# Performance work log

Hardware: AMD Instinct MI355X
Metric: run time of the kernel (lower is better)

## Reference

```python
import jax, jax.numpy as jnp
import numpy as np

M = 16            # num_frequencies
DIM = 512         # dim_input
B = 32768         # flattened batch
H = M + 1         # raw complex table side
N = 2 * M + 1     # autocorrelated table side
NPAR = H * H      # (m+1)^2


def setup_inputs() -> dict:
    key = jax.random.key(0)
    k1, k2, k3 = jax.random.split(key, 3)
    inputs = jax.random.normal(k1, (B, DIM), dtype=jnp.float32)
    targets = jax.random.uniform(k2, (B, 2), dtype=jnp.float32)  # points in [0,1) subset of [-1,1]^2
    # nn.init.normal_(weight, 0.01) => mean=0.01, std=1.0 ; bias zeros
    W = jax.random.normal(k3, (2 * NPAR, DIM), dtype=jnp.float32) + 0.01
    b = jnp.zeros((2 * NPAR,), dtype=jnp.float32)
    return {"inputs": inputs, "targets": targets, "W": W, "b": b}


def reference(inputs, targets, W, b):
    # Linear -> unconstrained complex (m+1)x(m+1) table per sample
    p = inputs @ W.T + b                                   # (B, 2*NPAR)
    real = p[:, :NPAR].reshape(-1, H, H)
    imag = p[:, NPAR:].reshape(-1, H, H)
    seq = jax.lax.complex(real, imag)                      # (B, H, H) complex64

    # 2D linear autocorrelation r[tau] = sum_i seq[i+tau] * conj(seq[i]),
    # tau in [-M, M]^2, via zero-padded FFT (equivalent to the grouped conv2d).
    F = jnp.fft.fft2(seq, s=(N, N))                        # (B, N, N)
    ac = jnp.fft.ifft2(F * jnp.conj(F))                    # circular autocorr
    ac = jnp.roll(ac, (M, M), axis=(-2, -1))               # index a -> lag a-M

    # Normalize so C[0,0] (= centre) equals 1/4 => unit mass on [-1,1]^2
    centre = ac[:, M, M].real                              # sum |seq|^2 > 0
    C = ac / (4.0 * centre)[:, None, None]                 # (B, N, N)

    # Evaluate f(x,y) = sum_{kx,ky} C * exp(i*pi*(kx*x + ky*y))
    k = jnp.arange(-M, M + 1, dtype=jnp.float32)
    kx, ky = jnp.meshgrid(k, k, indexing='xy')             # (N, N)
    tx = targets[:, 0][:, None, None]
    ty = targets[:, 1][:, None, None]
    phase = kx[None] * tx + ky[None] * ty                  # (B, N, N)
    exps = jnp.exp(1j * jnp.pi * phase)
    pdf = jnp.einsum('bij,bij->b', C, exps).real           # (B,)
    return pdf
```

## Files before the change

kernel.cpp:

```cpp
#include <hip/hip_runtime.h>

#define NPARC 289
#define NOUT  578
#define DIMK  512
#define BATCH 32768

typedef __bf16 bf16x8 __attribute__((ext_vector_type(8)));
typedef float floatx4 __attribute__((ext_vector_type(4)));

__device__ __forceinline__ unsigned short f2bf(float f) {
    unsigned u = __float_as_uint(f);
    u = (u + 0x7fffu + ((u >> 16) & 1u)) >> 16;
    return (unsigned short)u;
}

__global__ void prep_w(const float* __restrict__ W, unsigned short* __restrict__ Wp) {
    int wid = threadIdx.x >> 6;
    int lane = threadIdx.x & 63;
    int slot = blockIdx.x * 4 + wid;
    int k = lane * 8;
    unsigned short v[8];
    if (slot < NOUT) {
        int o = (slot & 1) ? NPARC + (slot >> 1) : (slot >> 1);
        const float* src = W + (size_t)o * DIMK + k;
        #pragma unroll
        for (int j = 0; j < 8; ++j) v[j] = f2bf(src[j]);
    } else {
        #pragma unroll
        for (int j = 0; j < 8; ++j) v[j] = 0;
    }
    int ct = slot >> 4;
    int ks = k >> 5;
    int ln = (((k >> 3) & 3) << 4) + (slot & 15);
    uint4 o4;
    o4.x = (unsigned)v[0] | ((unsigned)v[1] << 16);
    o4.y = (unsigned)v[2] | ((unsigned)v[3] << 16);
    o4.z = (unsigned)v[4] | ((unsigned)v[5] << 16);
    o4.w = (unsigned)v[6] | ((unsigned)v[7] << 16);
    *(uint4*)(Wp + (size_t)((ct * 16 + ks) * 64 + ln) * 8) = o4;
}

__global__ __launch_bounds__(512, 2) void fused_kernel(
    const float* __restrict__ inputs, const float* __restrict__ targets,
    const float* __restrict__ bias, const unsigned short* __restrict__ Wp,
    float* __restrict__ out)
{
    __shared__ __align__(16) float buf[2][64 * 128];
    __shared__ float R[8][64][3];
    const int tid  = threadIdx.x;
    const int base = blockIdx.x * 64;
    const int wid  = tid >> 6;
    const int lane = tid & 63;
    const int quad = lane >> 4;
    const int lcol = lane & 15;
    const int ct0  = wid * 5;
    const bf16x8* Wf = (const bf16x8*)Wp;

#define STAGE(nb, kt) do {                                                    \
    _Pragma("unroll") for (int j_ = 0; j_ < 4; ++j_) {                        \
        int I_ = wid * 4 + j_;                                                \
        int r_ = I_ * 2 + (lane >> 5);                                        \
        int cl_ = (lane & 31) ^ (r_ & 15);                                    \
        const float* g_ = inputs + (size_t)(base + r_) * DIMK + (kt) * 128 + cl_ * 4; \
        void* l_ = (char*)&buf[nb][0] + I_ * 1024;                            \
        __builtin_amdgcn_global_load_lds(                                     \
            (const __attribute__((address_space(1))) unsigned int*)g_,        \
            (__attribute__((address_space(3))) unsigned int*)l_, 16, 0, 0);   \
    }                                                                         \
} while (0)

#define LDRAW(R_, nb, kl) do {                                                \
    _Pragma("unroll") for (int st_ = 0; st_ < 4; ++st_) {                     \
        int s_ = st_ * 16 + lcol;                                             \
        int cb_ = (kl) * 8 + quad * 2;                                        \
        const char* p_ = (const char*)&buf[nb][0] + s_ * 512;                 \
        R_[2 * st_]     = *(const floatx4*)(p_ + ((cb_)     ^ (s_ & 15)) * 16); \
        R_[2 * st_ + 1] = *(const floatx4*)(p_ + ((cb_ + 1) ^ (s_ & 15)) * 16); \
    }                                                                         \
} while (0)

#define LDAW(dst, ksg)                                                        \
    { _Pragma("unroll") for (int t5_ = 0; t5_ < 5; ++t5_)                     \
        dst[t5_] = Wf[((size_t)(ct0 + t5_) * 16 + (ksg)) * 64 + lane]; }

#define KS(nb, ksg, RU, RP, PF, AWU, AWP) do {                                \
    if (PF) LDRAW(RP, nb, ((ksg) & 3) + 1);                                   \
    if ((ksg) < 15) LDAW(AWP, (ksg) + 1);                                     \
    bf16x8 bsv[4];                                                            \
    _Pragma("unroll") for (int st_ = 0; st_ < 4; ++st_) {                     \
        union { __bf16 h[8]; bf16x8 v; } cu_;                                 \
        cu_.h[0] = (__bf16)RU[2 * st_][0];     cu_.h[1] = (__bf16)RU[2 * st_][1]; \
        cu_.h[2] = (__bf16)RU[2 * st_][2];     cu_.h[3] = (__bf16)RU[2 * st_][3]; \
        cu_.h[4] = (__bf16)RU[2 * st_ + 1][0]; cu_.h[5] = (__bf16)RU[2 * st_ + 1][1]; \
        cu_.h[6] = (__bf16)RU[2 * st_ + 1][2]; cu_.h[7] = (__bf16)RU[2 * st_ + 1][3]; \
        bsv[st_] = cu_.v;                                                     \
    }                                                                         \
    __builtin_amdgcn_sched_barrier(0);                                        \
    __builtin_amdgcn_s_setprio(1);                                            \
    _Pragma("unroll") for (int t5_ = 0; t5_ < 5; ++t5_)                       \
        { _Pragma("unroll") for (int st_ = 0; st_ < 4; ++st_)                 \
            acc[t5_][st_] = __builtin_amdgcn_mfma_f32_16x16x32_bf16(          \
                AWU[t5_], bsv[st_], acc[t5_][st_], 0, 0, 0); }                \
    __builtin_amdgcn_s_setprio(0);                                            \
    __builtin_amdgcn_sched_barrier(0);                                        \
} while (0)

    floatx4 acc[5][4];
    #pragma unroll
    for (int t5 = 0; t5 < 5; ++t5)
        #pragma unroll
        for (int st = 0; st < 4; ++st) acc[t5][st] = (floatx4){0.f, 0.f, 0.f, 0.f};

    bf16x8 aw0[5], aw1[5];
    floatx4 rA[8], rB[8];

    STAGE(0, 0);
    LDAW(aw0, 0);
    __syncthreads();

    STAGE(1, 1);
    LDRAW(rA, 0, 0);
    KS(0, 0,  rA, rB, 1, aw0, aw1);
    KS(0, 1,  rB, rA, 1, aw1, aw0);
    KS(0, 2,  rA, rB, 1, aw0, aw1);
    KS(0, 3,  rB, rA, 0, aw1, aw0);
    __syncthreads();

    STAGE(0, 2);
    LDRAW(rA, 1, 0);
    KS(1, 4,  rA, rB, 1, aw0, aw1);
    KS(1, 5,  rB, rA, 1, aw1, aw0);
    KS(1, 6,  rA, rB, 1, aw0, aw1);
    KS(1, 7,  rB, rA, 0, aw1, aw0);
    __syncthreads();

    STAGE(1, 3);
    LDRAW(rA, 0, 0);
    KS(0, 8,  rA, rB, 1, aw0, aw1);
    KS(0, 9,  rB, rA, 1, aw1, aw0);
    KS(0, 10, rA, rB, 1, aw0, aw1);
    KS(0, 11, rB, rA, 0, aw1, aw0);
    __syncthreads();

    LDRAW(rA, 1, 0);
    KS(1, 12, rA, rB, 1, aw0, aw1);
    KS(1, 13, rB, rA, 1, aw1, aw0);
    KS(1, 14, rA, rB, 1, aw0, aw1);
    KS(1, 15, rB, rA, 0, aw1, aw0);

    float xs[4], ys[4];
    #pragma unroll
    for (int st = 0; st < 4; ++st) {
        float2 t2 = *(const float2*)(targets + 2 * (base + st * 16 + lcol));
        xs[st] = 0.5f * t2.x;
        ys[st] = 0.5f * t2.y;
    }

    float pd[4]  = {0.f, 0.f, 0.f, 0.f};
    float pr[4]  = {0.f, 0.f, 0.f, 0.f};
    float pim[4] = {0.f, 0.f, 0.f, 0.f};

    #pragma unroll
    for (int t5 = 0; t5 < 5; ++t5)
        #pragma unroll
        for (int p = 0; p < 2; ++p) {
            int colw = (ct0 + t5) * 16 + quad * 4 + 2 * p;
            if (colw < NOUT) {
                int jj = colw >> 1;
                int r = jj / 17;
                int c = jj - r * 17;
                float cf = (float)c, rf = (float)r;
                float be = bias[jj];
                float bo = bias[jj + NPARC];
                #pragma unroll
                for (int st = 0; st < 4; ++st) {
                    float ve = acc[t5][st][2 * p]     + be;
                    float vo = acc[t5][st][2 * p + 1] + bo;
                    float u = fmaf(cf, xs[st], rf * ys[st]);
                    u = __builtin_amdgcn_fractf(u);
                    float sn = __builtin_amdgcn_sinf(u);
                    float cs = __builtin_amdgcn_cosf(u);
                    pd[st]  = fmaf(ve, ve, pd[st]);
                    pd[st]  = fmaf(vo, vo, pd[st]);
                    pr[st]  = fmaf(ve, cs, pr[st]);
                    pr[st]  = fmaf(-vo, sn, pr[st]);
                    pim[st] = fmaf(ve, sn, pim[st]);
                    pim[st] = fmaf(vo, cs, pim[st]);
                }
            }
        }

    #pragma unroll
    for (int d = 16; d < 64; d <<= 1)
        #pragma unroll
        for (int st = 0; st < 4; ++st) {
            pd[st]  += __shfl_xor(pd[st], d, 64);
            pr[st]  += __shfl_xor(pr[st], d, 64);
            pim[st] += __shfl_xor(pim[st], d, 64);
        }

    if (lane < 16) {
        #pragma unroll
        for (int st = 0; st < 4; ++st) {
            int sl = st * 16 + lane;
            R[wid][sl][0] = pd[st];
            R[wid][sl][1] = pr[st];
            R[wid][sl][2] = pim[st];
        }
    }
    __syncthreads();

    if (tid < 64) {
        float sd = 0.f, sr = 0.f, si = 0.f;
        #pragma unroll
        for (int w = 0; w < 8; ++w) {
            sd += R[w][tid][0];
            sr += R[w][tid][1];
            si += R[w][tid][2];
        }
        out[base + tid] = (sr * sr + si * si) / (4.0f * sd);
    }
#undef STAGE
#undef LDRAW
#undef LDAW
#undef KS
}

extern "C" void kernel_launch(void* const* d_in, const int* in_sizes, int n_in,
                              void* d_out, int out_size, void* d_ws, size_t ws_size,
                              hipStream_t stream) {
    const float* inputs  = (const float*)d_in[0];
    const float* targets = (const float*)d_in[1];
    const float* W       = (const float*)d_in[2];
    const float* bias    = (const float*)d_in[3];
    unsigned short* Wp   = (unsigned short*)d_ws;

    prep_w<<<160, 256, 0, stream>>>(W, Wp);
    fused_kernel<<<BATCH / 64, 512, 0, stream>>>(inputs, targets, bias, Wp, (float*)d_out);
}
```

Baseline: 120.3 us.

## Stage inputs as bf16 in LDS via register prefetch and triple-buffered weights

Replaces the async global-to-LDS fp32 copy with register-staged global loads that convert the input tile to bf16 once per block before writing it to a half-size swizzled LDS buffer. MFMA operand reads then become single bf16x8 LDS loads with no per-step conversion, and weight fragments rotate through three register sets to prefetch two k-steps ahead. It also uses explicit lgkmcnt waits plus raw s_barrier in place of __syncthreads. The intent is to halve LDS footprint and traffic and remove redundant fp32-to-bf16 conversions done by every wave, at the cost of more VGPRs for the prefetched global data and extra weight buffers.

```diff
diff --git a/kernel.cpp b/kernel.cpp
--- a/kernel.cpp
+++ b/kernel.cpp
@@ -45,7 +45,7 @@
     const float* __restrict__ bias, const unsigned short* __restrict__ Wp,
     float* __restrict__ out)
 {
-    __shared__ __align__(16) float buf[2][64 * 128];
+    __shared__ __align__(16) unsigned short buf[2][1024][8];
     __shared__ float R[8][64][3];
     const int tid  = threadIdx.x;
     const int base = blockIdx.x * 64;
@@ -56,54 +56,62 @@
     const int ct0  = wid * 5;
     const bf16x8* Wf = (const bf16x8*)Wp;
 
-#define STAGE(nb, kt) do {                                                    \
-    _Pragma("unroll") for (int j_ = 0; j_ < 4; ++j_) {                        \
-        int I_ = wid * 4 + j_;                                                \
-        int r_ = I_ * 2 + (lane >> 5);                                        \
-        int cl_ = (lane & 31) ^ (r_ & 15);                                    \
-        const float* g_ = inputs + (size_t)(base + r_) * DIMK + (kt) * 128 + cl_ * 4; \
-        void* l_ = (char*)&buf[nb][0] + I_ * 1024;                            \
-        __builtin_amdgcn_global_load_lds(                                     \
-            (const __attribute__((address_space(1))) unsigned int*)g_,        \
-            (__attribute__((address_space(3))) unsigned int*)l_, 16, 0, 0);   \
-    }                                                                         \
+    const int rowA  = tid >> 4;
+    const int rowB  = 32 + (tid >> 4);
+    const int cch   = tid & 15;
+    const int physA = cch ^ (rowA & 15);
+    const int physB = cch ^ (rowB & 15);
+    const float* inb = inputs + (size_t)base * DIMK;
+
+    float4 ga0, ga1, gb0, gb1;
+
+#define GLOAD(t) do {                                                         \
+    const float* pA_ = inb + (size_t)rowA * DIMK + (t) * 128 + cch * 8;       \
+    const float* pB_ = inb + (size_t)rowB * DIMK + (t) * 128 + cch * 8;       \
+    ga0 = *(const float4*)pA_; ga1 = *(const float4*)(pA_ + 4);               \
+    gb0 = *(const float4*)pB_; gb1 = *(const float4*)(pB_ + 4);               \
 } while (0)
 
-#define LDRAW(R_, nb, kl) do {                                                \
-    _Pragma("unroll") for (int st_ = 0; st_ < 4; ++st_) {                     \
-        int s_ = st_ * 16 + lcol;                                             \
-        int cb_ = (kl) * 8 + quad * 2;                                        \
-        const char* p_ = (const char*)&buf[nb][0] + s_ * 512;                 \
-        R_[2 * st_]     = *(const floatx4*)(p_ + ((cb_)     ^ (s_ & 15)) * 16); \
-        R_[2 * st_ + 1] = *(const floatx4*)(p_ + ((cb_ + 1) ^ (s_ & 15)) * 16); \
-    }                                                                         \
+#define CVTWRITE(nb) do {                                                     \
+    union { __bf16 h[8]; uint4 u; } cA_, cB_;                                 \
+    cA_.h[0]=(__bf16)ga0.x; cA_.h[1]=(__bf16)ga0.y;                           \
+    cA_.h[2]=(__bf16)ga0.z; cA_.h[3]=(__bf16)ga0.w;                           \
+    cA_.h[4]=(__bf16)ga1.x; cA_.h[5]=(__bf16)ga1.y;                           \
+    cA_.h[6]=(__bf16)ga1.z; cA_.h[7]=(__bf16)ga1.w;                           \
+    cB_.h[0]=(__bf16)gb0.x; cB_.h[1]=(__bf16)gb0.y;                           \
+    cB_.h[2]=(__bf16)gb0.z; cB_.h[3]=(__bf16)gb0.w;                           \
+    cB_.h[4]=(__bf16)gb1.x; cB_.h[5]=(__bf16)gb1.y;                           \
+    cB_.h[6]=(__bf16)gb1.z; cB_.h[7]=(__bf16)gb1.w;                           \
+    *(uint4*)&buf[nb][rowA * 16 + physA][0] = cA_.u;                          \
+    *(uint4*)&buf[nb][rowB * 16 + physB][0] = cB_.u;                          \
 } while (0)
 
 #define LDAW(dst, ksg)                                                        \
     { _Pragma("unroll") for (int t5_ = 0; t5_ < 5; ++t5_)                     \
         dst[t5_] = Wf[((size_t)(ct0 + t5_) * 16 + (ksg)) * 64 + lane]; }
 
-#define KS(nb, ksg, RU, RP, PF, AWU, AWP) do {                                \
-    if (PF) LDRAW(RP, nb, ((ksg) & 3) + 1);                                   \
-    if ((ksg) < 15) LDAW(AWP, (ksg) + 1);                                     \
-    bf16x8 bsv[4];                                                            \
-    _Pragma("unroll") for (int st_ = 0; st_ < 4; ++st_) {                     \
-        union { __bf16 h[8]; bf16x8 v; } cu_;                                 \
-        cu_.h[0] = (__bf16)RU[2 * st_][0];     cu_.h[1] = (__bf16)RU[2 * st_][1]; \
-        cu_.h[2] = (__bf16)RU[2 * st_][2];     cu_.h[3] = (__bf16)RU[2 * st_][3]; \
-        cu_.h[4] = (__bf16)RU[2 * st_ + 1][0]; cu_.h[5] = (__bf16)RU[2 * st_ + 1][1]; \
-        cu_.h[6] = (__bf16)RU[2 * st_ + 1][2]; cu_.h[7] = (__bf16)RU[2 * st_ + 1][3]; \
-        bsv[st_] = cu_.v;                                                     \
-    }                                                                         \
+#define LDBS(dst, nb, jl)                                                     \
+    { _Pragma("unroll") for (int st_ = 0; st_ < 4; ++st_) {                   \
+        int sr_ = st_ * 16 + lcol;                                            \
+        dst[st_] = *(const bf16x8*)&buf[nb][sr_ * 16 +                        \
+                       (((jl) * 4 + quad) ^ (sr_ & 15))][0]; }  }
+
+#define MFMA20(AW, BS)                                                        \
     __builtin_amdgcn_sched_barrier(0);                                        \
     __builtin_amdgcn_s_setprio(1);                                            \
-    _Pragma("unroll") for (int t5_ = 0; t5_ < 5; ++t5_)                       \
-        { _Pragma("unroll") for (int st_ = 0; st_ < 4; ++st_)                 \
-            acc[t5_][st_] = __builtin_amdgcn_mfma_f32_16x16x32_bf16(          \
-                AWU[t5_], bsv[st_], acc[t5_][st_], 0, 0, 0); }                \
+    { _Pragma("unroll") for (int t5_ = 0; t5_ < 5; ++t5_)                     \
+      { _Pragma("unroll") for (int st_ = 0; st_ < 4; ++st_)                   \
+          acc[t5_][st_] = __builtin_amdgcn_mfma_f32_16x16x32_bf16(            \
+              AW[t5_], BS[st_], acc[t5_][st_], 0, 0, 0); } }                  \
     __builtin_amdgcn_s_setprio(0);                                            \
+    __builtin_amdgcn_sched_barrier(0);
+
+#define BARRIER_LGKM()                                                        \
     __builtin_amdgcn_sched_barrier(0);                                        \
-} while (0)
+    asm volatile("s_waitcnt lgkmcnt(0)" ::: "memory");                        \
+    __builtin_amdgcn_sched_barrier(0);                                        \
+    __builtin_amdgcn_s_barrier();                                             \
+    __builtin_amdgcn_sched_barrier(0);
 
     floatx4 acc[5][4];
     #pragma unroll
@@ -111,42 +119,46 @@
         #pragma unroll
         for (int st = 0; st < 4; ++st) acc[t5][st] = (floatx4){0.f, 0.f, 0.f, 0.f};
 
-    bf16x8 aw0[5], aw1[5];
-    floatx4 rA[8], rB[8];
-
-    STAGE(0, 0);
-    LDAW(aw0, 0);
+    bf16x8 a0[5], a1[5], a2[5], bsA[4], bsB[4];
+
+    LDAW(a0, 0);
+    LDAW(a1, 1);
+    GLOAD(0);
+    CVTWRITE(0);
     __syncthreads();
 
-    STAGE(1, 1);
-    LDRAW(rA, 0, 0);
-    KS(0, 0,  rA, rB, 1, aw0, aw1);
-    KS(0, 1,  rB, rA, 1, aw1, aw0);
-    KS(0, 2,  rA, rB, 1, aw0, aw1);
-    KS(0, 3,  rB, rA, 0, aw1, aw0);
-    __syncthreads();
-
-    STAGE(0, 2);
-    LDRAW(rA, 1, 0);
-    KS(1, 4,  rA, rB, 1, aw0, aw1);
-    KS(1, 5,  rB, rA, 1, aw1, aw0);
-    KS(1, 6,  rA, rB, 1, aw0, aw1);
-    KS(1, 7,  rB, rA, 0, aw1, aw0);
-    __syncthreads();
-
-    STAGE(1, 3);
-    LDRAW(rA, 0, 0);
-    KS(0, 8,  rA, rB, 1, aw0, aw1);
-    KS(0, 9,  rB, rA, 1, aw1, aw0);
-    KS(0, 10, rA, rB, 1, aw0, aw1);
-    KS(0, 11, rB, rA, 0, aw1, aw0);
-    __syncthreads();
-
-    LDRAW(rA, 1, 0);
-    KS(1, 12, rA, rB, 1, aw0, aw1);
-    KS(1, 13, rB, rA, 1, aw1, aw0);
-    KS(1, 14, rA, rB, 1, aw0, aw1);
-    KS(1, 15, rB, rA, 0, aw1, aw0);
+    GLOAD(1);
+    LDBS(bsA, 0, 0);
+    LDAW(a2, 2);  LDBS(bsB, 0, 1);  MFMA20(a0, bsA);
+    LDAW(a0, 3);  LDBS(bsA, 0, 2);  MFMA20(a1, bsB);
+    LDAW(a1, 4);  LDBS(bsB, 0, 3);  MFMA20(a2, bsA);
+    LDAW(a2, 5);                    MFMA20(a0, bsB);
+    CVTWRITE(1);
+    BARRIER_LGKM();
+
+    GLOAD(2);
+    LDBS(bsA, 1, 0);
+    LDAW(a0, 6);  LDBS(bsB, 1, 1);  MFMA20(a1, bsA);
+    LDAW(a1, 7);  LDBS(bsA, 1, 2);  MFMA20(a2, bsB);
+    LDAW(a2, 8);  LDBS(bsB, 1, 3);  MFMA20(a0, bsA);
+    LDAW(a0, 9);                    MFMA20(a1, bsB);
+    CVTWRITE(0);
+    BARRIER_LGKM();
+
+    GLOAD(3);
+    LDBS(bsA, 0, 0);
+    LDAW(a1, 10); LDBS(bsB, 0, 1);  MFMA20(a2, bsA);
+    LDAW(a2, 11); LDBS(bsA, 0, 2);  MFMA20(a0, bsB);
+    LDAW(a0, 12); LDBS(bsB, 0, 3);  MFMA20(a1, bsA);
+    LDAW(a1, 13);                   MFMA20(a2, bsB);
+    CVTWRITE(1);
+    BARRIER_LGKM();
+
+    LDBS(bsA, 1, 0);
+    LDAW(a2, 14); LDBS(bsB, 1, 1);  MFMA20(a0, bsA);
+    LDAW(a0, 15); LDBS(bsA, 1, 2);  MFMA20(a1, bsB);
+                  LDBS(bsB, 1, 3);  MFMA20(a2, bsA);
+                                    MFMA20(a0, bsB);
 
     float xs[4], ys[4];
     #pragma unroll
@@ -220,10 +232,12 @@
         }
         out[base + tid] = (sr * sr + si * si) / (4.0f * sd);
     }
-#undef STAGE
-#undef LDRAW
+#undef GLOAD
+#undef CVTWRITE
 #undef LDAW
-#undef KS
+#undef LDBS
+#undef MFMA20
+#undef BARRIER_LGKM
 }
 
 extern "C" void kernel_launch(void* const* d_in, const int* in_sizes, int n_in,
```

Measured after the change: 115.3 us. 4.1% less time.
